# Performance work log

Hardware: AMD Instinct MI355X
Metric: run time of the kernel (lower is better)

## Reference

```python
import jax, jax.numpy as jnp
import numpy as np
import math

N_HEAD = 16
HEAD_QKV = 1024  # total qkv width; head_dim = HEAD_QKV // N_HEAD
WM_DECAY_LENGTH = 2048
WM_DECAY_RATE = 1.0
WM_ECHOIC = 16


def decay_weight_matrix(n):
    # power_law decay, faithful to get_decay_weight_matrix
    dl = WM_DECAY_LENGTH - WM_ECHOIC + 1
    nums = jnp.linspace(0.0, 1.0, dl)
    decay_values = 1.0 - jnp.power(nums, 1.0 / (np.e * WM_DECAY_RATE))
    decay_values = jnp.concatenate([jnp.ones(WM_ECHOIC - 1), decay_values])  # [WM_DECAY_LENGTH]
    decay_values = decay_values[:n]
    idx = jnp.arange(n)[:, None] - jnp.arange(n)[None, :]  # [n,n], negative above diag
    mat = decay_values[jnp.clip(idx, 0, n - 1)]
    return jnp.tril(mat).astype(jnp.float32)


def setup_inputs() -> dict:
    key = jax.random.key(0)
    k1, k2, k3 = jax.random.split(key, 3)
    B, T, C = 2, 2048, 1024
    x = jax.random.normal(k1, (B, T, C), dtype=jnp.float32)
    W_attn = jax.random.normal(k2, (C, 3 * HEAD_QKV), dtype=jnp.float32) * (1.0 / math.sqrt(C))
    W_proj = jax.random.normal(k3, (HEAD_QKV, C), dtype=jnp.float32) * (1.0 / math.sqrt(HEAD_QKV))
    return {"x": x, "W_attn": W_attn, "W_proj": W_proj}


def reference(x, W_attn, W_proj):
    B, T, C = x.shape
    hd = HEAD_QKV // N_HEAD
    qkv = x @ W_attn  # [B,T,3*HEAD_QKV]
    q, k, v = jnp.split(qkv, 3, axis=-1)
    # [B,T,HQKV] -> [B,H,T,hd]
    q = q.reshape(B, T, N_HEAD, hd).transpose(0, 2, 1, 3)
    k = k.reshape(B, T, N_HEAD, hd).transpose(0, 2, 1, 3)
    v = v.reshape(B, T, N_HEAD, hd).transpose(0, 2, 1, 3)
    att = jnp.einsum('bhqd,bhkd->bhqk', q, k) * (1.0 / math.sqrt(hd))
    causal = jnp.tril(jnp.ones((T, T), dtype=bool))
    att = jnp.where(causal, att, -jnp.inf)
    att = jax.nn.softmax(att, axis=-1)
    att = att * decay_weight_matrix(T)  # post-softmax multiplicative decay
    y = jnp.einsum('bhqk,bhkd->bhqd', att, v)
    y = y.transpose(0, 2, 1, 3).reshape(B, T, HEAD_QKV)
    return y @ W_proj
```

## Files before the change

kernel.cpp:

```cpp
#include <hip/hip_runtime.h>
#include <math.h>

#define B_  2
#define T_  2048
#define C_  1024
#define NH_ 16
#define HD_ 64
#define N3_ 3072

typedef float f32x4 __attribute__((ext_vector_type(4)));
typedef short bf16x8 __attribute__((ext_vector_type(8)));
typedef unsigned short u16;

#define QSCALE 0.18033688011112042f

#if __has_builtin(__builtin_amdgcn_exp2f)
#define EXP2(x) __builtin_amdgcn_exp2f(x)
#else
#define EXP2(x) exp2f(x)
#endif

__device__ __forceinline__ u16 f2bf(float x) {
  unsigned int u = __builtin_bit_cast(unsigned int, x);
  u += 0x7FFFu + ((u >> 16) & 1u);
  return (u16)(u >> 16);
}

__device__ __forceinline__ unsigned int cvt_pk_bf16(float lo, float hi) {
  unsigned int r;
  asm("v_cvt_pk_bf16_f32 %0, %1, %2" : "=v"(r) : "v"(lo), "v"(hi));
  return r;
}

#define GLD16(g, l) __builtin_amdgcn_global_load_lds( \
    (__attribute__((address_space(1))) void*)(g), \
    (__attribute__((address_space(3))) void*)(l), 16, 0, 0)

__global__ __launch_bounds__(256) void cvt4_kernel(const float* __restrict__ in,
                                                   u16* __restrict__ out, int n) {
  int i = (blockIdx.x * 256 + threadIdx.x) * 4;
  if (i >= n) return;
  float4 v = *(const float4*)(in + i);
  ushort4 o;
  o.x = f2bf(v.x); o.y = f2bf(v.y); o.z = f2bf(v.z); o.w = f2bf(v.w);
  *(ushort4*)(out + i) = o;
}

__global__ __launch_bounds__(256) void transpose_cvt_kernel(const float* __restrict__ in,
                                                            u16* __restrict__ out,
                                                            int R, int Cc) {
  __shared__ float tile[32][33];
  int c0 = blockIdx.x * 32, r0 = blockIdx.y * 32;
  int tx = threadIdx.x & 31, ty = threadIdx.x >> 5;
#pragma unroll
  for (int rr = ty; rr < 32; rr += 8)
    tile[rr][tx] = in[(size_t)(r0 + rr) * Cc + c0 + tx];
  __syncthreads();
#pragma unroll
  for (int rr = ty; rr < 32; rr += 8)
    out[(size_t)(c0 + rr) * R + r0 + tx] = f2bf(tile[tx][rr]);
}

__global__ __launch_bounds__(256) void decay_init_kernel(float* __restrict__ decayp) {
  int i = blockIdx.x * 256 + threadIdx.x;
  if (i >= 2176) return;
  int d = i - 128;
  float v = 1.0f;
  if (d >= 15) v = 1.0f - powf((float)(d - 15) * (1.0f / 2032.0f), 0.36787944117144233f);
  decayp[i] = v;
}

__global__ __launch_bounds__(256) void vtrans_kernel(const u16* __restrict__ V,
                                                     u16* __restrict__ VT) {
  __shared__ u16 tile[64][72];
  int bh = blockIdx.y, t0 = blockIdx.x * 64;
  const u16* src = V + ((size_t)bh * T_ + t0) * HD_;
  int r = threadIdx.x >> 2;
  int c8 = (threadIdx.x & 3) * 16;
  *(bf16x8*)(&tile[r][c8])     = *(const bf16x8*)(src + (size_t)r * HD_ + c8);
  *(bf16x8*)(&tile[r][c8 + 8]) = *(const bf16x8*)(src + (size_t)r * HD_ + c8 + 8);
  __syncthreads();
  int d = threadIdx.x >> 2;
  int tc = (threadIdx.x & 3) * 16;
  u16 outv[16];
#pragma unroll
  for (int j = 0; j < 16; ++j) outv[j] = tile[tc + j][d];
  u16* dst = VT + ((size_t)bh * HD_ + d) * T_ + t0 + tc;
  *(bf16x8*)(dst)     = *(bf16x8*)(outv);
  *(bf16x8*)(dst + 8) = *(bf16x8*)(outv + 8);
}

template<int MODE>
__global__ __launch_bounds__(256, 3) void gemm128_kernel(
    const u16* __restrict__ A, const u16* __restrict__ Bt,
    float* __restrict__ Cf, u16* __restrict__ Cq, u16* __restrict__ Vt,
    int M, int N, int K)
{
  __shared__ char lds[32768];
  const int lane = threadIdx.x & 63;
  const int wave = threadIdx.x >> 6;
  const int m0 = blockIdx.y << 7;
  const int n0 = blockIdx.x << 7;
  const int wm = wave >> 1, wn = wave & 1;

  f32x4 acc[4][4] = {};

#define GSTAGE(buf, k0)                                                          \
  {                                                                              \
    _Pragma("unroll")                                                            \
    for (int c = 0; c < 2; ++c) {                                                \
      int chunk = wave * 2048 + c * 1024;                                        \
      int row = (chunk >> 6) + (lane >> 2);                                      \
      int wb = ((lane & 3) << 4) ^ ((row & 3) << 4);                             \
      GLD16((const char*)(A  + (size_t)(m0 + row) * K + (k0)) + wb,              \
            lds + (buf) * 16384 + chunk);                                        \
      GLD16((const char*)(Bt + (size_t)(n0 + row) * K + (k0)) + wb,              \
            lds + (buf) * 16384 + 8192 + chunk);                                 \
    }                                                                            \
  }

  GSTAGE(0, 0);
  __syncthreads();

  for (int k0 = 0; k0 < K; k0 += 32) {
    const int cur = (k0 >> 5) & 1;
    if (k0 + 32 < K) GSTAGE(cur ^ 1, k0 + 32);
    const char* base = lds + cur * 16384;
    bf16x8 af[4], bfr[4];
#pragma unroll
    for (int m = 0; m < 4; ++m) {
      int row = wm * 64 + m * 16 + (lane & 15);
      int wb = ((lane >> 4) << 4) ^ ((row & 3) << 4);
      af[m] = *(const bf16x8*)(base + row * 64 + wb);
    }
#pragma unroll
    for (int n = 0; n < 4; ++n) {
      int row = wn * 64 + n * 16 + (lane & 15);
      int wb = ((lane >> 4) << 4) ^ ((row & 3) << 4);
      bfr[n] = *(const bf16x8*)(base + 8192 + row * 64 + wb);
    }
    __builtin_amdgcn_s_setprio(1);
#pragma unroll
    for (int m = 0; m < 4; ++m)
#pragma unroll
      for (int n = 0; n < 4; ++n)
        acc[m][n] = __builtin_amdgcn_mfma_f32_16x16x32_bf16(af[m], bfr[n], acc[m][n], 0, 0, 0);
    __builtin_amdgcn_s_setprio(0);
    __syncthreads();
  }

#pragma unroll
  for (int m = 0; m < 4; ++m) {
    int grow0 = m0 + wm * 64 + m * 16 + ((lane >> 4) << 2);
#pragma unroll
    for (int n = 0; n < 4; ++n) {
      int gcol = n0 + wn * 64 + n * 16 + (lane & 15);
      f32x4 v = acc[m][n];
#pragma unroll
      for (int r = 0; r < 4; ++r) {
        int grow = grow0 + r;
        if (MODE == 0) {
          int bb = grow >> 11, tt = grow & 2047;
          int which = gcol >> 10, rem = gcol & 1023;
          int hh = rem >> 6, dd = rem & 63;
          if (which < 2) {
            float ov = (which == 0) ? v[r] * QSCALE : v[r];
            Cq[((size_t)(which * 32 + bb * 16 + hh) * 2048 + tt) * 64 + dd] = f2bf(ov);
          } else {
            Vt[((size_t)(bb * 16 + hh) * 2048 + tt) * 64 + dd] = f2bf(v[r]);
          }
        } else {
          Cf[(size_t)grow * N + gcol] = v[r];
        }
      }
    }
  }
#undef GSTAGE
}

__global__ __launch_bounds__(256, 2) void attn_kernel(
    const u16* __restrict__ qkb, const u16* __restrict__ vtg,
    const float* __restrict__ decayg,
    u16* __restrict__ yb)
{
  __shared__ char klds[2][8192];
  __shared__ char vlds[2][8192];
  __shared__ u16 plds[128 * 76];

  const int lane = threadIdx.x & 63;
  const int wave = threadIdx.x >> 6;
  const int quad = lane >> 4;
  const int l15 = lane & 15;
  const int qtA = blockIdx.x;
  const int qtB = 31 - qtA;
  const int bh = blockIdx.y;
  const int b = bh >> 4, h = bh & 15;

  const u16* Q   = qkb + (size_t)bh * T_ * HD_;
  const u16* Kg  = qkb + (size_t)(32 + bh) * T_ * HD_;
  const u16* VTg = vtg + (size_t)bh * HD_ * T_;

  const int wrowB = qtB * 64 + wave * 16;
  const int wrowA = qtA * 64 + wave * 16;
  const int qB = wrowB + l15;
  const int qA = wrowA + l15;
  const int qBq = qB - quad * 4;
  const int qAq = qA - quad * 4;

  bf16x8 qaB[2], qaA[2];
  { const u16* qp = Q + (size_t)(wrowB + l15) * HD_ + quad * 8;
    qaB[0] = *(const bf16x8*)qp; qaB[1] = *(const bf16x8*)(qp + 32); }
  { const u16* qp = Q + (size_t)(wrowA + l15) * HD_ + quad * 8;
    qaA[0] = *(const bf16x8*)qp; qaA[1] = *(const bf16x8*)(qp + 32); }

  f32x4 accB[4] = {}, accA[4] = {};
  float lsumB = 0.0f, lsumA = 0.0f;

#define ASTAGE(buf, kt)                                                          \
  {                                                                              \
    _Pragma("unroll")                                                            \
    for (int c = 0; c < 2; ++c) {                                                \
      int chunk = wave * 2048 + c * 1024;                                        \
      int row = (chunk >> 7) + (lane >> 3);                                      \
      int wb = ((lane & 7) << 4) ^ ((row & 7) << 4);                             \
      GLD16((const char*)(Kg + (size_t)((kt) * 64 + row) * HD_) + wb,            \
            klds[buf] + chunk);                                                  \
      GLD16((const char*)(VTg + (size_t)row * T_ + (kt) * 64) + wb,              \
            vlds[buf] + chunk);                                                  \
    }                                                                            \
  }

  ASTAGE(0, 0);
  __syncthreads();

  const int nkt = qtB + 1;
  for (int kt = 0; kt < nkt; ++kt) {
    const int cur = kt & 1;
    if (kt + 1 < nkt) ASTAGE(cur ^ 1, kt + 1);
    const bool actA = (kt <= qtA);

    bf16x8 kf[4][2];
#pragma unroll
    for (int f = 0; f < 4; ++f) {
      int krow = f * 16 + l15;
      int base = krow * 128;
      int msk = (krow & 7) << 4;
      kf[f][0] = *(const bf16x8*)(klds[cur] + base + ((quad * 16) ^ msk));
      kf[f][1] = *(const bf16x8*)(klds[cur] + base + ((64 + quad * 16) ^ msk));
    }

    f32x4 sB[4], sA[4];
    __builtin_amdgcn_s_setprio(1);
#pragma unroll
    for (int f = 0; f < 4; ++f) {
      f32x4 t = {};
      t = __builtin_amdgcn_mfma_f32_16x16x32_bf16(kf[f][0], qaB[0], t, 0, 0, 0);
      t = __builtin_amdgcn_mfma_f32_16x16x32_bf16(kf[f][1], qaB[1], t, 0, 0, 0);
      sB[f] = t;
    }
    if (actA) {
#pragma unroll
      for (int f = 0; f < 4; ++f) {
        f32x4 t = {};
        t = __builtin_amdgcn_mfma_f32_16x16x32_bf16(kf[f][0], qaA[0], t, 0, 0, 0);
        t = __builtin_amdgcn_mfma_f32_16x16x32_bf16(kf[f][1], qaA[1], t, 0, 0, 0);
        sA[f] = t;
      }
    }
    __builtin_amdgcn_s_setprio(0);

    if (kt == qtB) {
#pragma unroll
      for (int f = 0; f < 4; ++f) {
        int key0 = kt * 64 + f * 16 + quad * 4;
#pragma unroll
        for (int r = 0; r < 4; ++r)
          if (key0 + r > qB) sB[f][r] = -1e30f;
      }
    }
    if (actA && kt == qtA) {
#pragma unroll
      for (int f = 0; f < 4; ++f) {
        int key0 = kt * 64 + f * 16 + quad * 4;
#pragma unroll
        for (int r = 0; r < 4; ++r)
          if (key0 + r > qA) sA[f][r] = -1e30f;
      }
    }

    {
      const float* db = decayg + (qBq - kt * 64);
#pragma unroll
      for (int f = 0; f < 4; ++f) {
        f32x4 p;
#pragma unroll
        for (int r = 0; r < 4; ++r) p[r] = EXP2(sB[f][r]);
        lsumB += (p[0] + p[1]) + (p[2] + p[3]);
        const float* dbf = db - f * 16;
        unsigned int w0 = cvt_pk_bf16(p[0] * dbf[0],  p[1] * dbf[-1]);
        unsigned int w1 = cvt_pk_bf16(p[2] * dbf[-2], p[3] * dbf[-3]);
        uint2 wv; wv.x = w0; wv.y = w1;
        *(uint2*)(plds + (size_t)(wave * 16 + l15) * 76 + f * 16 + quad * 4) = wv;
      }
    }
    if (actA) {
      const float* db = decayg + (qAq - kt * 64);
#pragma unroll
      for (int f = 0; f < 4; ++f) {
        f32x4 p;
#pragma unroll
        for (int r = 0; r < 4; ++r) p[r] = EXP2(sA[f][r]);
        lsumA += (p[0] + p[1]) + (p[2] + p[3]);
        const float* dbf = db - f * 16;
        unsigned int w0 = cvt_pk_bf16(p[0] * dbf[0],  p[1] * dbf[-1]);
        unsigned int w1 = cvt_pk_bf16(p[2] * dbf[-2], p[3] * dbf[-3]);
        uint2 wv; wv.x = w0; wv.y = w1;
        *(uint2*)(plds + (size_t)(64 + wave * 16 + l15) * 76 + f * 16 + quad * 4) = wv;
      }
    }

    bf16x8 vf[4][2];
#pragma unroll
    for (int n = 0; n < 4; ++n) {
      int vrow = n * 16 + l15;
      int mskv = (vrow & 7) << 4;
#pragma unroll
      for (int ks = 0; ks < 2; ++ks)
        vf[n][ks] = *(const bf16x8*)(vlds[cur] + vrow * 128 + ((ks * 64 + quad * 16) ^ mskv));
    }

    __builtin_amdgcn_s_setprio(1);
#pragma unroll
    for (int ks = 0; ks < 2; ++ks) {
      bf16x8 pa = *(const bf16x8*)(plds + (size_t)(wave * 16 + l15) * 76 + ks * 32 + quad * 8);
#pragma unroll
      for (int n = 0; n < 4; ++n)
        accB[n] = __builtin_amdgcn_mfma_f32_16x16x32_bf16(pa, vf[n][ks], accB[n], 0, 0, 0);
    }
    if (actA) {
#pragma unroll
      for (int ks = 0; ks < 2; ++ks) {
        bf16x8 pa = *(const bf16x8*)(plds + (size_t)(64 + wave * 16 + l15) * 76 + ks * 32 + quad * 8);
#pragma unroll
        for (int n = 0; n < 4; ++n)
          accA[n] = __builtin_amdgcn_mfma_f32_16x16x32_bf16(pa, vf[n][ks], accA[n], 0, 0, 0);
      }
    }
    __builtin_amdgcn_s_setprio(0);
    __syncthreads();
  }
#undef ASTAGE

  lsumB += __shfl_xor(lsumB, 16); lsumB += __shfl_xor(lsumB, 32);
  lsumA += __shfl_xor(lsumA, 16); lsumA += __shfl_xor(lsumA, 32);
  float rB[4], rA[4];
#pragma unroll
  for (int r = 0; r < 4; ++r) {
    rB[r] = 1.0f / __shfl(lsumB, quad * 4 + r, 16);
    rA[r] = 1.0f / __shfl(lsumA, quad * 4 + r, 16);
  }
#pragma unroll
  for (int n = 0; n < 4; ++n) {
    int d = h * 64 + n * 16 + l15;
#pragma unroll
    for (int r = 0; r < 4; ++r) {
      int tB = wrowB + quad * 4 + r;
      int tA = wrowA + quad * 4 + r;
      yb[((size_t)b * T_ + tB) * 1024 + d] = f2bf(accB[n][r] * rB[r]);
      yb[((size_t)b * T_ + tA) * 1024 + d] = f2bf(accA[n][r] * rA[r]);
    }
  }
}

extern "C" void kernel_launch(void* const* d_in, const int* in_sizes, int n_in,
                              void* d_out, int out_size, void* d_ws, size_t ws_size,
                              hipStream_t stream) {
  const float* x  = (const float*)d_in[0];
  const float* Wa = (const float*)d_in[1];
  const float* Wp = (const float*)d_in[2];
  float* out = (float*)d_out;
  char* ws = (char*)d_ws;

  u16*   xb    = (u16*)(ws + 0);
  u16*   WaT   = (u16*)(ws + 8388608);
  u16*   WpT   = (u16*)(ws + 14680064);
  u16*   qkb   = (u16*)(ws + 16777216);
  u16*   Vtmp  = (u16*)(ws + 33554432);
  u16*   VT    = (u16*)(ws + 41943040);
  float* decayp = (float*)Vtmp;
  u16*   yb    = xb;

  cvt4_kernel<<<4096, 256, 0, stream>>>(x, xb, B_ * T_ * C_);
  transpose_cvt_kernel<<<dim3(96, 32), 256, 0, stream>>>(Wa, WaT, C_, N3_);
  transpose_cvt_kernel<<<dim3(32, 32), 256, 0, stream>>>(Wp, WpT, C_, C_);

  gemm128_kernel<0><<<dim3(N3_ / 128, 32), 256, 0, stream>>>(
      xb, WaT, nullptr, qkb, Vtmp, B_ * T_, N3_, C_);
  vtrans_kernel<<<dim3(32, 32), 256, 0, stream>>>(Vtmp, VT);
  decay_init_kernel<<<9, 256, 0, stream>>>(decayp);
  attn_kernel<<<dim3(16, 32), 256, 0, stream>>>(qkb, VT, decayp + 128, yb);
  gemm128_kernel<1><<<dim3(1024 / 128, 32), 256, 0, stream>>>(
      yb, WpT, out, nullptr, nullptr, B_ * T_, 1024, 1024);
}
```

Measured before the change: 121.8 us.

## Remap blocks across XCDs, reverse decay table for vector loads, raise attn occupancy

New measurement: 120.7 us. Within noise of the previous version (-0.8%).

```diff
diff --git a/kernel.cpp b/kernel.cpp
--- a/kernel.cpp
+++ b/kernel.cpp
@@ -11,6 +11,8 @@
 typedef float f32x4 __attribute__((ext_vector_type(4)));
 typedef short bf16x8 __attribute__((ext_vector_type(8)));
 typedef unsigned short u16;
+typedef float f32x4_base __attribute__((ext_vector_type(4)));
+typedef f32x4_base __attribute__((aligned(4))) f32x4u;
 
 #define QSCALE 0.18033688011112042f
 
@@ -61,13 +63,13 @@
     out[(size_t)(c0 + rr) * R + r0 + tx] = f2bf(tile[tx][rr]);
 }
 
-__global__ __launch_bounds__(256) void decay_init_kernel(float* __restrict__ decayp) {
-  int i = blockIdx.x * 256 + threadIdx.x;
-  if (i >= 2176) return;
-  int d = i - 128;
+__global__ __launch_bounds__(256) void decay_init_kernel(float* __restrict__ decR) {
+  int j = blockIdx.x * 256 + threadIdx.x;
+  if (j >= 2176) return;
+  int d = 2047 - j;
   float v = 1.0f;
   if (d >= 15) v = 1.0f - powf((float)(d - 15) * (1.0f / 2032.0f), 0.36787944117144233f);
-  decayp[i] = v;
+  decR[j] = v;
 }
 
 __global__ __launch_bounds__(256) void vtrans_kernel(const u16* __restrict__ V,
@@ -99,8 +101,12 @@
   __shared__ char lds[32768];
   const int lane = threadIdx.x & 63;
   const int wave = threadIdx.x >> 6;
-  const int m0 = blockIdx.y << 7;
-  const int n0 = blockIdx.x << 7;
+  const int nxb = N >> 7;
+  const int orig = blockIdx.x;
+  const int cpx = (int)gridDim.x >> 3;
+  const int wg = (orig & 7) * cpx + (orig >> 3);
+  const int m0 = (wg / nxb) << 7;
+  const int n0 = (wg % nxb) << 7;
   const int wm = wave >> 1, wn = wave & 1;
 
   f32x4 acc[4][4] = {};
@@ -178,10 +184,9 @@
 #undef GSTAGE
 }
 
-__global__ __launch_bounds__(256, 2) void attn_kernel(
+__global__ __launch_bounds__(256, 3) void attn_kernel(
     const u16* __restrict__ qkb, const u16* __restrict__ vtg,
-    const float* __restrict__ decayg,
-    u16* __restrict__ yb)
+    const float* __restrict__ decR, u16* __restrict__ yb)
 {
   __shared__ char klds[2][8192];
   __shared__ char vlds[2][8192];
@@ -191,9 +196,11 @@
   const int wave = threadIdx.x >> 6;
   const int quad = lane >> 4;
   const int l15 = lane & 15;
-  const int qtA = blockIdx.x;
+  const int orig = blockIdx.x;
+  const int wg = ((orig & 7) << 6) + (orig >> 3);
+  const int qtA = wg & 15;
   const int qtB = 31 - qtA;
-  const int bh = blockIdx.y;
+  const int bh = wg >> 4;
   const int b = bh >> 4, h = bh & 15;
 
   const u16* Q   = qkb + (size_t)bh * T_ * HD_;
@@ -204,8 +211,8 @@
   const int wrowA = qtA * 64 + wave * 16;
   const int qB = wrowB + l15;
   const int qA = wrowA + l15;
-  const int qBq = qB - quad * 4;
-  const int qAq = qA - quad * 4;
+  const int rbase0B = 2047 - qB + quad * 4;
+  const int rbase0A = 2047 - qA + quad * 4;
 
   bf16x8 qaB[2], qaA[2];
   { const u16* qp = Q + (size_t)(wrowB + l15) * HD_ + quad * 8;
@@ -249,6 +256,16 @@
       kf[f][1] = *(const bf16x8*)(klds[cur] + base + ((64 + quad * 16) ^ msk));
     }
 
+    const float* dRB = decR + (rbase0B + kt * 64);
+    const float* dRA = decR + (rbase0A + kt * 64);
+    f32x4 dB[4], dA[4];
+#pragma unroll
+    for (int f = 0; f < 4; ++f) dB[f] = *(const f32x4u*)(dRB + f * 16);
+    if (actA) {
+#pragma unroll
+      for (int f = 0; f < 4; ++f) dA[f] = *(const f32x4u*)(dRA + f * 16);
+    }
+
     f32x4 sB[4], sA[4];
     __builtin_amdgcn_s_setprio(1);
 #pragma unroll
@@ -288,32 +305,26 @@
       }
     }
 
-    {
-      const float* db = decayg + (qBq - kt * 64);
+#pragma unroll
+    for (int f = 0; f < 4; ++f) {
+      f32x4 p;
+#pragma unroll
+      for (int r = 0; r < 4; ++r) p[r] = EXP2(sB[f][r]);
+      lsumB += (p[0] + p[1]) + (p[2] + p[3]);
+      unsigned int w0 = cvt_pk_bf16(p[0] * dB[f][0], p[1] * dB[f][1]);
+      unsigned int w1 = cvt_pk_bf16(p[2] * dB[f][2], p[3] * dB[f][3]);
+      uint2 wv; wv.x = w0; wv.y = w1;
+      *(uint2*)(plds + (size_t)(wave * 16 + l15) * 76 + f * 16 + quad * 4) = wv;
+    }
+    if (actA) {
 #pragma unroll
       for (int f = 0; f < 4; ++f) {
         f32x4 p;
 #pragma unroll
-        for (int r = 0; r < 4; ++r) p[r] = EXP2(sB[f][r]);
-        lsumB += (p[0] + p[1]) + (p[2] + p[3]);
-        const float* dbf = db - f * 16;
-        unsigned int w0 = cvt_pk_bf16(p[0] * dbf[0],  p[1] * dbf[-1]);
-        unsigned int w1 = cvt_pk_bf16(p[2] * dbf[-2], p[3] * dbf[-3]);
-        uint2 wv; wv.x = w0; wv.y = w1;
-        *(uint2*)(plds + (size_t)(wave * 16 + l15) * 76 + f * 16 + quad * 4) = wv;
-      }
-    }
-    if (actA) {
-      const float* db = decayg + (qAq - kt * 64);
-#pragma unroll
-      for (int f = 0; f < 4; ++f) {
-        f32x4 p;
-#pragma unroll
         for (int r = 0; r < 4; ++r) p[r] = EXP2(sA[f][r]);
         lsumA += (p[0] + p[1]) + (p[2] + p[3]);
-        const float* dbf = db - f * 16;
-        unsigned int w0 = cvt_pk_bf16(p[0] * dbf[0],  p[1] * dbf[-1]);
-        unsigned int w1 = cvt_pk_bf16(p[2] * dbf[-2], p[3] * dbf[-3]);
+        unsigned int w0 = cvt_pk_bf16(p[0] * dA[f][0], p[1] * dA[f][1]);
+        unsigned int w1 = cvt_pk_bf16(p[2] * dA[f][2], p[3] * dA[f][3]);
         uint2 wv; wv.x = w0; wv.y = w1;
         *(uint2*)(plds + (size_t)(64 + wave * 16 + l15) * 76 + f * 16 + quad * 4) = wv;
       }
@@ -387,18 +398,18 @@
   u16*   qkb   = (u16*)(ws + 16777216);
   u16*   Vtmp  = (u16*)(ws + 33554432);
   u16*   VT    = (u16*)(ws + 41943040);
-  float* decayp = (float*)Vtmp;
+  float* decR  = (float*)Vtmp;
   u16*   yb    = xb;
 
   cvt4_kernel<<<4096, 256, 0, stream>>>(x, xb, B_ * T_ * C_);
   transpose_cvt_kernel<<<dim3(96, 32), 256, 0, stream>>>(Wa, WaT, C_, N3_);
   transpose_cvt_kernel<<<dim3(32, 32), 256, 0, stream>>>(Wp, WpT, C_, C_);
 
-  gemm128_kernel<0><<<dim3(N3_ / 128, 32), 256, 0, stream>>>(
+  gemm128_kernel<0><<<768, 256, 0, stream>>>(
       xb, WaT, nullptr, qkb, Vtmp, B_ * T_, N3_, C_);
   vtrans_kernel<<<dim3(32, 32), 256, 0, stream>>>(Vtmp, VT);
-  decay_init_kernel<<<9, 256, 0, stream>>>(decayp);
-  attn_kernel<<<dim3(16, 32), 256, 0, stream>>>(qkb, VT, decayp + 128, yb);
-  gemm128_kernel<1><<<dim3(1024 / 128, 32), 256, 0, stream>>>(
+  decay_init_kernel<<<9, 256, 0, stream>>>(decR);
+  attn_kernel<<<512, 256, 0, stream>>>(qkb, VT, decR, yb);
+  gemm128_kernel<1><<<256, 256, 0, stream>>>(
       yb, WpT, out, nullptr, nullptr, B_ * T_, 1024, 1024);
 }
```
